# Optimization experiments

Hardware: AMD Instinct MI355X
Metric: run time of the kernel (lower is better)

The kernel has to match this reference:

```python
import jax, jax.numpy as jnp
import numpy as np

B, T, D_MODEL, N_HEADS, D_FF = 2, 2048, 512, 8, 2048
D_HEAD = D_MODEL // N_HEADS
EPS_LN = 1e-5
DEN_MIN = 1e-6


def setup_inputs() -> dict:
    key = jax.random.key(0)
    ks = jax.random.split(key, 12)
    def lin_w(k, din, dout):
        return jax.random.normal(k, (din, dout), jnp.float32) / np.sqrt(din).astype(np.float32)
    return {
        "x": jax.random.normal(ks[0], (B, T, D_MODEL), jnp.float32),
        "ln1_g": jnp.ones((D_MODEL,), jnp.float32),
        "ln1_b": jnp.zeros((D_MODEL,), jnp.float32),
        "Wq": lin_w(ks[1], D_MODEL, D_MODEL), "bq": jnp.zeros((D_MODEL,), jnp.float32),
        "Wk": lin_w(ks[2], D_MODEL, D_MODEL), "bk": jnp.zeros((D_MODEL,), jnp.float32),
        "Wv": lin_w(ks[3], D_MODEL, D_MODEL), "bv": jnp.zeros((D_MODEL,), jnp.float32),
        "Wo": lin_w(ks[4], D_MODEL, D_MODEL), "bo": jnp.zeros((D_MODEL,), jnp.float32),
        "ln2_g": jnp.ones((D_MODEL,), jnp.float32),
        "ln2_b": jnp.zeros((D_MODEL,), jnp.float32),
        "W1": lin_w(ks[5], D_MODEL, D_FF), "b1": jnp.zeros((D_FF,), jnp.float32),
        "W2": lin_w(ks[6], D_FF, D_MODEL), "b2": jnp.zeros((D_MODEL,), jnp.float32),
    }


def layer_norm(x, g, b):
    mu = jnp.mean(x, axis=-1, keepdims=True)
    var = jnp.var(x, axis=-1, keepdims=True)
    return (x - mu) * jax.lax.rsqrt(var + EPS_LN) * g + b


def causal_linear_attention(Q, K, V):
    # Q,K,V: (B,H,T,D); feature map already applied to Q,K.
    # Running summary S_t = cumsum_j phi(K_j) outer V_j, shape (B,H,T,D,D)
    KV = jnp.cumsum(K[..., :, None] * V[..., None, :], axis=2)
    z = jnp.cumsum(K, axis=2)                                   # (B,H,T,D)
    num = jnp.einsum('bhtd,bhtdm->bhtm', Q, KV)                 # (B,H,T,D)
    den = jnp.maximum(jnp.einsum('bhtd,bhtd->bht', Q, z), DEN_MIN)[..., None]
    return num / den


def reference(x, ln1_g, ln1_b, Wq, bq, Wk, bk, Wv, bv, Wo, bo,
              ln2_g, ln2_b, W1, b1, W2, b2):
    Bx, Tx, _ = x.shape
    # --- sublayer 1: pre-norm causal linear attention + residual ---
    h = layer_norm(x, ln1_g, ln1_b)
    def heads(y):  # (B,T,D_MODEL) -> (B,H,T,D_HEAD)
        return y.reshape(Bx, Tx, N_HEADS, D_HEAD).transpose(0, 2, 1, 3)
    Q = jax.nn.elu(heads(h @ Wq + bq)) + 1.0
    K = jax.nn.elu(heads(h @ Wk + bk)) + 1.0
    V = heads(h @ Wv + bv)
    attn = causal_linear_attention(Q, K, V)                     # (B,H,T,D)
    attn = attn.transpose(0, 2, 1, 3).reshape(Bx, Tx, D_MODEL)
    x = x + (attn @ Wo + bo)
    # --- sublayer 2: pre-norm FFN + residual (dropout=0, eval mode) ---
    h2 = layer_norm(x, ln2_g, ln2_b)
    ffn = jax.nn.relu(h2 @ W1 + b1) @ W2 + b2
    return x + ffn
```

## Files before the change

kernel.cpp:

```cpp
#include <hip/hip_runtime.h>
#include <hip/hip_bf16.h>
#include <cstdint>

#define T_SEQ   2048
#define DM      512
#define NH      8
#define DH      64
#define BATCH   2
#define MROWS   4096
#define DFF     2048
#define CHUNK   64
#define NCHUNK  32
#define BHN     16
#define ST_STRIDE 4160

typedef __attribute__((ext_vector_type(8))) short bf16x8;
typedef __attribute__((ext_vector_type(4))) float f32x4;
typedef __hip_bfloat16 bf16;

__device__ __forceinline__ void g2lds16(const bf16* g, bf16* l) {
    __builtin_amdgcn_global_load_lds(
        (const __attribute__((address_space(1))) unsigned int*)g,
        (__attribute__((address_space(3))) unsigned int*)l, 16, 0, 0);
}

__global__ __launch_bounds__(128) void ln_kernel(
    const float* __restrict__ x, const float* __restrict__ g,
    const float* __restrict__ b, bf16* __restrict__ y)
{
    int row = blockIdx.x;
    int t = threadIdx.x;
    const float4* xr = (const float4*)(x + (size_t)row * DM);
    float4 v = xr[t];
    float s  = v.x + v.y + v.z + v.w;
    float s2 = v.x*v.x + v.y*v.y + v.z*v.z + v.w*v.w;
#pragma unroll
    for (int off = 32; off > 0; off >>= 1) {
        s  += __shfl_down(s,  off);
        s2 += __shfl_down(s2, off);
    }
    __shared__ float sh[4];
    if ((t & 63) == 0) { sh[(t >> 6) * 2] = s; sh[(t >> 6) * 2 + 1] = s2; }
    __syncthreads();
    s  = sh[0] + sh[2];
    s2 = sh[1] + sh[3];
    float mu  = s * (1.0f / DM);
    float var = s2 * (1.0f / DM) - mu * mu;
    float rs  = rsqrtf(var + 1e-5f);
    float4 gg = ((const float4*)g)[t];
    float4 bb = ((const float4*)b)[t];
    union { short4 s4; bf16 h[4]; } u;
    u.h[0] = __float2bfloat16((v.x - mu) * rs * gg.x + bb.x);
    u.h[1] = __float2bfloat16((v.y - mu) * rs * gg.y + bb.y);
    u.h[2] = __float2bfloat16((v.z - mu) * rs * gg.z + bb.z);
    u.h[3] = __float2bfloat16((v.w - mu) * rs * gg.w + bb.w);
    *(short4*)(y + (size_t)row * DM + t * 4) = u.s4;
}

__global__ __launch_bounds__(256) void wcvt_all(
    const float* __restrict__ Wq, const float* __restrict__ Wk,
    const float* __restrict__ Wv, const float* __restrict__ Wo,
    const float* __restrict__ W1, const float* __restrict__ W2,
    bf16* __restrict__ QKVWT, bf16* __restrict__ WoT,
    bf16* __restrict__ W1T, bf16* __restrict__ W2T)
{
    __shared__ float tile[64][65];
    int bid = blockIdx.x;
    const float* src; bf16* dst; int K, N, txi, tyi;
    if (bid < 256) {
        int m = bid >> 6, t = bid & 63;
        src = m == 0 ? Wq : m == 1 ? Wk : m == 2 ? Wv : Wo;
        dst = m == 0 ? QKVWT : m == 1 ? QKVWT + 512*512
            : m == 2 ? QKVWT + 1024*512 : WoT;
        K = 512; N = 512; txi = t & 7; tyi = t >> 3;
    } else if (bid < 512) {
        int t = bid - 256;
        src = W1; dst = W1T; K = 512; N = 2048; txi = t & 31; tyi = t >> 5;
    } else {
        int t = bid - 512;
        src = W2; dst = W2T; K = 2048; N = 512; txi = t & 7; tyi = t >> 3;
    }
    int k0 = tyi * 64, n0 = txi * 64;
    int tid = threadIdx.x;
    int tr = tid >> 4, tc = (tid & 15) * 4;
#pragma unroll
    for (int i = 0; i < 4; i++) {
        float4 v = *(const float4*)(src + (size_t)(k0 + tr + i*16) * N + n0 + tc);
        tile[tr + i*16][tc+0] = v.x; tile[tr + i*16][tc+1] = v.y;
        tile[tr + i*16][tc+2] = v.z; tile[tr + i*16][tc+3] = v.w;
    }
    __syncthreads();
#pragma unroll
    for (int i = 0; i < 4; i++) {
        int n = tr + i*16;
        union { short4 s4; bf16 h[4]; } u;
#pragma unroll
        for (int j = 0; j < 4; j++) u.h[j] = __float2bfloat16(tile[tc+j][n]);
        *(short4*)(dst + (size_t)(n0 + n) * K + k0 + tc) = u.s4;
    }
}

template<int BM, int BN, int MODE>
__global__ __launch_bounds__(256) void mfma_gemm(
    const bf16* __restrict__ A, const bf16* __restrict__ Bt,
    const float* __restrict__ bias0, const float* __restrict__ bias1,
    const float* __restrict__ bias2, const float* __restrict__ res,
    float* __restrict__ outF,
    float* __restrict__ outQ, float* __restrict__ outK, float* __restrict__ outV,
    bf16* __restrict__ outB, int M, int N, int K)
{
    constexpr int BK = 64;
    constexpr int WTM = BM / 2, WTN = BN / 2;
    constexpr int FM = WTM / 16, FN = WTN / 16;
    __shared__ bf16 As[BM * BK];
    __shared__ bf16 Bs[BN * BK];
    const int tid = threadIdx.x;
    const int w = tid >> 6, lane = tid & 63;
    const int wr = w >> 1, wc = w & 1;
    const int bm0 = blockIdx.y * BM, bn0 = blockIdx.x * BN;
    const int srow = lane >> 3;
    const int scol = (lane & 7) * 8;

    f32x4 acc[FM][FN];
#pragma unroll
    for (int m = 0; m < FM; m++)
#pragma unroll
        for (int n = 0; n < FN; n++) acc[m][n] = (f32x4){0.f,0.f,0.f,0.f};

    for (int k0 = 0; k0 < K; k0 += BK) {
#pragma unroll
        for (int i = 0; i < BM/32; i++) {
            int c = i*4 + w;
            g2lds16(A + (size_t)(bm0 + c*8 + srow) * K + k0 + scol, &As[c*512]);
        }
#pragma unroll
        for (int i = 0; i < BN/32; i++) {
            int c = i*4 + w;
            g2lds16(Bt + (size_t)(bn0 + c*8 + srow) * K + k0 + scol, &Bs[c*512]);
        }
        __syncthreads();
#pragma unroll
        for (int kk = 0; kk < 2; kk++) {
            bf16x8 af[FM], bfr[FN];
#pragma unroll
            for (int m = 0; m < FM; m++)
                af[m] = *(const bf16x8*)&As[(wr*WTM + m*16 + (lane&15))*BK + kk*32 + (lane>>4)*8];
#pragma unroll
            for (int n = 0; n < FN; n++)
                bfr[n] = *(const bf16x8*)&Bs[(wc*WTN + n*16 + (lane&15))*BK + kk*32 + (lane>>4)*8];
#pragma unroll
            for (int m = 0; m < FM; m++)
#pragma unroll
                for (int n = 0; n < FN; n++)
                    acc[m][n] = __builtin_amdgcn_mfma_f32_16x16x32_bf16(af[m], bfr[n], acc[m][n], 0, 0, 0);
        }
        __syncthreads();
    }

    const int lr = (lane >> 4) * 4;
    const int lc = lane & 15;
#pragma unroll
    for (int m = 0; m < FM; m++) {
#pragma unroll
        for (int n = 0; n < FN; n++) {
            int col = bn0 + wc*WTN + n*16 + lc;
#pragma unroll
            for (int j = 0; j < 4; j++) {
                int r = bm0 + wr*WTM + m*16 + lr + j;
                float v = acc[m][n][j];
                if (MODE == 0) {
                    int which = col >> 9;
                    int cc = col & 511;
                    float bv_ = which == 0 ? bias0[cc] : which == 1 ? bias1[cc] : bias2[cc];
                    v += bv_;
                    if (which < 2) v = v > 0.f ? v + 1.f : __expf(v);
                    int hh = cc >> 6, dd = cc & 63;
                    int bb = r >> 11, tt = r & 2047;
                    float* dst = which == 0 ? outQ : which == 1 ? outK : outV;
                    dst[((((size_t)(bb*NH + hh)) * T_SEQ + tt) << 6) + dd] = v;
                } else if (MODE == 1) {
                    v += bias0[col] + res[(size_t)r * N + col];
                    outF[(size_t)r * N + col] = v;
                } else {
                    v += bias0[col];
                    v = fmaxf(v, 0.f);
                    outB[(size_t)r * N + col] = __float2bfloat16(v);
                }
            }
        }
    }
}

__global__ __launch_bounds__(256) void attn_chunk_sum(
    const float* __restrict__ Kb, const float* __restrict__ Vb,
    float* __restrict__ St)
{
    int blk = blockIdx.x;
    const float* Kp = Kb + (size_t)blk * (CHUNK * DH);
    const float* Vp = Vb + (size_t)blk * (CHUNK * DH);
    float* Sp = St + (size_t)blk * ST_STRIDE;
    __shared__ float Ks[64][64];
    __shared__ float Vs[64][64];
    int tid = threadIdx.x;
#pragma unroll
    for (int i = 0; i < 4; i++) {
        ((float4*)Ks)[tid + i*256] = ((const float4*)Kp)[tid + i*256];
        ((float4*)Vs)[tid + i*256] = ((const float4*)Vp)[tid + i*256];
    }
    __syncthreads();
    int r  = tid >> 2;
    int c0 = (tid & 3) * 16;
    float s[16];
#pragma unroll
    for (int i = 0; i < 16; i++) s[i] = 0.0f;
    for (int t = 0; t < 64; t++) {
        float kv = Ks[t][r];
        const float4* vr = (const float4*)&Vs[t][c0];
        float4 v0 = vr[0], v1 = vr[1], v2 = vr[2], v3 = vr[3];
        s[0]+=kv*v0.x; s[1]+=kv*v0.y; s[2]+=kv*v0.z; s[3]+=kv*v0.w;
        s[4]+=kv*v1.x; s[5]+=kv*v1.y; s[6]+=kv*v1.z; s[7]+=kv*v1.w;
        s[8]+=kv*v2.x; s[9]+=kv*v2.y; s[10]+=kv*v2.z; s[11]+=kv*v2.w;
        s[12]+=kv*v3.x; s[13]+=kv*v3.y; s[14]+=kv*v3.z; s[15]+=kv*v3.w;
    }
#pragma unroll
    for (int i = 0; i < 4; i++) {
        float4 ov = make_float4(s[i*4+0], s[i*4+1], s[i*4+2], s[i*4+3]);
        *(float4*)(Sp + (size_t)r*64 + c0 + i*4) = ov;
    }
    if (tid < 64) {
        float z = 0.0f;
        for (int t = 0; t < 64; t++) z += Ks[t][tid];
        Sp[4096 + tid] = z;
    }
}

__global__ __launch_bounds__(64) void attn_scan(float* __restrict__ St)
{
    int f4 = blockIdx.x * 64 + threadIdx.x;
    if (f4 >= ST_STRIDE / 4) return;
    int bh = blockIdx.y;
    float4* base = (float4*)(St + (size_t)bh * NCHUNK * ST_STRIDE) + f4;
    float4 run = make_float4(0.f, 0.f, 0.f, 0.f);
#pragma unroll 4
    for (int ch = 0; ch < NCHUNK; ch++) {
        float4* p = base + (size_t)ch * (ST_STRIDE / 4);
        float4 t = *p;
        *p = run;
        run.x += t.x; run.y += t.y; run.z += t.z; run.w += t.w;
    }
}

__global__ __launch_bounds__(256) void attn_out_k(
    const float* __restrict__ Qb, const float* __restrict__ Kb,
    const float* __restrict__ Vb, const float* __restrict__ St,
    bf16* __restrict__ attnb)
{
    int blk = blockIdx.x;
    int bh = blk >> 5, ch = blk & 31;
    int b = bh >> 3, h = bh & 7;
    const float* Qp = Qb + (size_t)blk * 4096;
    const float* Kp = Kb + (size_t)blk * 4096;
    const float* Vp = Vb + (size_t)blk * 4096;
    const float* Sp = St + (size_t)blk * ST_STRIDE;
    __shared__ float Qs[64][68];
    __shared__ float Kt[64][68];
    __shared__ float Vs[64][68];
    __shared__ float Ss[64][68];
    __shared__ float Amat[64][65];
    __shared__ float zs[64];
    int tid = threadIdx.x;
#pragma unroll
    for (int i = 0; i < 4; i++) {
        int fi = tid + i*256;
        int t  = fi >> 4;
        int d4 = (fi & 15) * 4;
        float4 q = ((const float4*)Qp)[fi];
        float4 k = ((const float4*)Kp)[fi];
        float4 v = ((const float4*)Vp)[fi];
        float4 s = ((const float4*)Sp)[fi];
        *(float4*)&Qs[t][d4] = q;
        *(float4*)&Vs[t][d4] = v;
        *(float4*)&Ss[t][d4] = s;
        Kt[d4+0][t] = k.x; Kt[d4+1][t] = k.y; Kt[d4+2][t] = k.z; Kt[d4+3][t] = k.w;
    }
    if (tid < 64) zs[tid] = Sp[4096 + tid];
    __syncthreads();
    int r  = tid >> 2;
    int c0 = (tid & 3) * 16;
    float a[16];
#pragma unroll
    for (int i = 0; i < 16; i++) a[i] = 0.0f;
    for (int d = 0; d < 64; d++) {
        float q = Qs[r][d];
        const float4* kr = (const float4*)&Kt[d][c0];
        float4 k0 = kr[0], k1 = kr[1], k2 = kr[2], k3 = kr[3];
        a[0]+=q*k0.x; a[1]+=q*k0.y; a[2]+=q*k0.z; a[3]+=q*k0.w;
        a[4]+=q*k1.x; a[5]+=q*k1.y; a[6]+=q*k1.z; a[7]+=q*k1.w;
        a[8]+=q*k2.x; a[9]+=q*k2.y; a[10]+=q*k2.z; a[11]+=q*k2.w;
        a[12]+=q*k3.x; a[13]+=q*k3.y; a[14]+=q*k3.z; a[15]+=q*k3.w;
    }
#pragma unroll
    for (int i = 0; i < 16; i++) Amat[r][c0+i] = a[i];
    __syncthreads();
    float den = 0.0f;
    for (int d = 0; d < 64; d++) den += Qs[r][d] * zs[d];
    for (int j = 0; j <= r; j++) den += Amat[r][j];
    den = fmaxf(den, 1e-6f);
    float num[16];
#pragma unroll
    for (int i = 0; i < 16; i++) num[i] = 0.0f;
    for (int d = 0; d < 64; d++) {
        float q = Qs[r][d];
        const float4* sv = (const float4*)&Ss[d][c0];
        float4 s0 = sv[0], s1 = sv[1], s2 = sv[2], s3 = sv[3];
        num[0]+=q*s0.x; num[1]+=q*s0.y; num[2]+=q*s0.z; num[3]+=q*s0.w;
        num[4]+=q*s1.x; num[5]+=q*s1.y; num[6]+=q*s1.z; num[7]+=q*s1.w;
        num[8]+=q*s2.x; num[9]+=q*s2.y; num[10]+=q*s2.z; num[11]+=q*s2.w;
        num[12]+=q*s3.x; num[13]+=q*s3.y; num[14]+=q*s3.z; num[15]+=q*s3.w;
    }
    for (int j = 0; j <= r; j++) {
        float aj = Amat[r][j];
        const float4* vv = (const float4*)&Vs[j][c0];
        float4 v0 = vv[0], v1 = vv[1], v2 = vv[2], v3 = vv[3];
        num[0]+=aj*v0.x; num[1]+=aj*v0.y; num[2]+=aj*v0.z; num[3]+=aj*v0.w;
        num[4]+=aj*v1.x; num[5]+=aj*v1.y; num[6]+=aj*v1.z; num[7]+=aj*v1.w;
        num[8]+=aj*v2.x; num[9]+=aj*v2.y; num[10]+=aj*v2.z; num[11]+=aj*v2.w;
        num[12]+=aj*v3.x; num[13]+=aj*v3.y; num[14]+=aj*v3.z; num[15]+=aj*v3.w;
    }
    float inv = 1.0f / den;
    union { short4 s4[4]; bf16 hh[16]; } u;
#pragma unroll
    for (int i = 0; i < 16; i++) u.hh[i] = __float2bfloat16(num[i] * inv);
    short4* op = (short4*)(attnb + ((size_t)b * T_SEQ + ch*64 + r) * DM + h*64 + c0);
#pragma unroll
    for (int i = 0; i < 4; i++) op[i] = u.s4[i];
}

extern "C" void kernel_launch(void* const* d_in, const int* in_sizes, int n_in,
                              void* d_out, int out_size, void* d_ws, size_t ws_size,
                              hipStream_t stream)
{
    (void)in_sizes; (void)n_in; (void)out_size; (void)ws_size;
    const float* x     = (const float*)d_in[0];
    const float* ln1_g = (const float*)d_in[1];
    const float* ln1_b = (const float*)d_in[2];
    const float* Wq = (const float*)d_in[3];
    const float* bq = (const float*)d_in[4];
    const float* Wk = (const float*)d_in[5];
    const float* bk = (const float*)d_in[6];
    const float* Wv = (const float*)d_in[7];
    const float* bv = (const float*)d_in[8];
    const float* Wo = (const float*)d_in[9];
    const float* bo = (const float*)d_in[10];
    const float* ln2_g = (const float*)d_in[11];
    const float* ln2_b = (const float*)d_in[12];
    const float* W1 = (const float*)d_in[13];
    const float* b1 = (const float*)d_in[14];
    const float* W2 = (const float*)d_in[15];
    const float* b2 = (const float*)d_in[16];
    float* out = (float*)d_out;
    char* base = (char*)d_ws;

    bf16*  h_bf  = (bf16*)(base + 0);
    bf16*  h2_bf = (bf16*)(base + 4194304);
    bf16*  attnb = (bf16*)(base + 8388608);
    bf16*  QKVWT = (bf16*)(base + 12582912);
    bf16*  WoT   = (bf16*)(base + 14155776);
    bf16*  W1T   = (bf16*)(base + 14680064);
    bf16*  W2T   = (bf16*)(base + 16777216);
    float* Qb    = (float*)(base + 18874368);
    float* Kb    = (float*)(base + 27262976);
    float* Vb    = (float*)(base + 35651584);
    float* St    = (float*)(base + 44040192);
    float* X2    = (float*)(base + 52559872);
    bf16*  FF    = (bf16*)(base + 60948480);

    wcvt_all<<<768, 256, 0, stream>>>(Wq, Wk, Wv, Wo, W1, W2,
                                      QKVWT, WoT, W1T, W2T);

    ln_kernel<<<MROWS, 128, 0, stream>>>(x, ln1_g, ln1_b, h_bf);

    mfma_gemm<128,128,0><<<dim3(12, 32), 256, 0, stream>>>(
        h_bf, QKVWT, bq, bk, bv, nullptr, nullptr, Qb, Kb, Vb, nullptr,
        MROWS, 1536, 512);

    attn_chunk_sum<<<BHN*NCHUNK, 256, 0, stream>>>(Kb, Vb, St);
    attn_scan<<<dim3(17, BHN), 64, 0, stream>>>(St);
    attn_out_k<<<BHN*NCHUNK, 256, 0, stream>>>(Qb, Kb, Vb, St, attnb);

    mfma_gemm<64,128,1><<<dim3(4, 64), 256, 0, stream>>>(
        attnb, WoT, bo, nullptr, nullptr, x, X2, nullptr, nullptr, nullptr, nullptr,
        MROWS, 512, 512);

    ln_kernel<<<MROWS, 128, 0, stream>>>(X2, ln2_g, ln2_b, h2_bf);

    mfma_gemm<128,128,2><<<dim3(16, 32), 256, 0, stream>>>(
        h2_bf, W1T, b1, nullptr, nullptr, nullptr, nullptr, nullptr, nullptr, nullptr, FF,
        MROWS, DFF, 512);

    mfma_gemm<64,128,1><<<dim3(4, 64), 256, 0, stream>>>(
        FF, W2T, b2, nullptr, nullptr, X2, out, nullptr, nullptr, nullptr, nullptr,
        MROWS, 512, DFF);
}
```

Measured before the change: 233.0 us.

## Split-K final FFN GEMM with atomics, retile GEMMs with configurable wave layouts

The GEMM template now takes a configurable wave grid, so the QKV and W1 GEMMs run with 8 waves (512 threads) and the Wo GEMM uses 64x64 tiles to launch more blocks. The W2 GEMM is split along K into two halves and accumulates into the output with atomic adds. The second layernorm kernel pre-initialises the output with residual plus b2 so those atomics can land on it. This aims to raise occupancy and block count on the small-N GEMMs, at the cost of atomic traffic and floating-point summation that is no longer deterministic.

After: 228.7 us. About the same (-1.9%).

```diff
diff --git a/kernel.cpp b/kernel.cpp
--- a/kernel.cpp
+++ b/kernel.cpp
@@ -24,9 +24,11 @@
         (__attribute__((address_space(3))) unsigned int*)l, 16, 0, 0);
 }
 
+template<bool INIT>
 __global__ __launch_bounds__(128) void ln_kernel(
     const float* __restrict__ x, const float* __restrict__ g,
-    const float* __restrict__ b, bf16* __restrict__ y)
+    const float* __restrict__ b, bf16* __restrict__ y,
+    const float* __restrict__ b2, float* __restrict__ oinit)
 {
     int row = blockIdx.x;
     int t = threadIdx.x;
@@ -55,6 +57,11 @@
     u.h[2] = __float2bfloat16((v.z - mu) * rs * gg.z + bb.z);
     u.h[3] = __float2bfloat16((v.w - mu) * rs * gg.w + bb.w);
     *(short4*)(y + (size_t)row * DM + t * 4) = u.s4;
+    if (INIT) {
+        float4 b2v = ((const float4*)b2)[t];
+        float4 ov = make_float4(v.x + b2v.x, v.y + b2v.y, v.z + b2v.z, v.w + b2v.w);
+        ((float4*)(oinit + (size_t)row * DM))[t] = ov;
+    }
 }
 
 __global__ __launch_bounds__(256) void wcvt_all(
@@ -100,8 +107,8 @@
     }
 }
 
-template<int BM, int BN, int MODE>
-__global__ __launch_bounds__(256) void mfma_gemm(
+template<int BM, int BN, int WM, int WN, int MODE>
+__global__ __launch_bounds__(WM*WN*64) void mfma_gemm(
     const bf16* __restrict__ A, const bf16* __restrict__ Bt,
     const float* __restrict__ bias0, const float* __restrict__ bias1,
     const float* __restrict__ bias2, const float* __restrict__ res,
@@ -110,32 +117,37 @@
     bf16* __restrict__ outB, int M, int N, int K)
 {
     constexpr int BK = 64;
-    constexpr int WTM = BM / 2, WTN = BN / 2;
+    constexpr int WAVES = WM * WN;
+    constexpr int WTM = BM / WM, WTN = BN / WN;
     constexpr int FM = WTM / 16, FN = WTN / 16;
+    constexpr int IA = BM / 8 / WAVES, IB = BN / 8 / WAVES;
     __shared__ bf16 As[BM * BK];
     __shared__ bf16 Bs[BN * BK];
     const int tid = threadIdx.x;
     const int w = tid >> 6, lane = tid & 63;
-    const int wr = w >> 1, wc = w & 1;
+    const int wr = w / WN, wc = w % WN;
     const int bm0 = blockIdx.y * BM, bn0 = blockIdx.x * BN;
     const int srow = lane >> 3;
     const int scol = (lane & 7) * 8;
 
+    int kbeg = 0, kend = K;
+    if (MODE == 3) { int half = K >> 1; kbeg = blockIdx.z * half; kend = kbeg + half; }
+
     f32x4 acc[FM][FN];
 #pragma unroll
     for (int m = 0; m < FM; m++)
 #pragma unroll
         for (int n = 0; n < FN; n++) acc[m][n] = (f32x4){0.f,0.f,0.f,0.f};
 
-    for (int k0 = 0; k0 < K; k0 += BK) {
-#pragma unroll
-        for (int i = 0; i < BM/32; i++) {
-            int c = i*4 + w;
+    for (int k0 = kbeg; k0 < kend; k0 += BK) {
+#pragma unroll
+        for (int i = 0; i < IA; i++) {
+            int c = i*WAVES + w;
             g2lds16(A + (size_t)(bm0 + c*8 + srow) * K + k0 + scol, &As[c*512]);
         }
 #pragma unroll
-        for (int i = 0; i < BN/32; i++) {
-            int c = i*4 + w;
+        for (int i = 0; i < IB; i++) {
+            int c = i*WAVES + w;
             g2lds16(Bt + (size_t)(bn0 + c*8 + srow) * K + k0 + scol, &Bs[c*512]);
         }
         __syncthreads();
@@ -181,10 +193,12 @@
                 } else if (MODE == 1) {
                     v += bias0[col] + res[(size_t)r * N + col];
                     outF[(size_t)r * N + col] = v;
-                } else {
+                } else if (MODE == 2) {
                     v += bias0[col];
                     v = fmaxf(v, 0.f);
                     outB[(size_t)r * N + col] = __float2bfloat16(v);
+                } else {
+                    unsafeAtomicAdd(&outF[(size_t)r * N + col], v);
                 }
             }
         }
@@ -378,9 +392,9 @@
     wcvt_all<<<768, 256, 0, stream>>>(Wq, Wk, Wv, Wo, W1, W2,
                                       QKVWT, WoT, W1T, W2T);
 
-    ln_kernel<<<MROWS, 128, 0, stream>>>(x, ln1_g, ln1_b, h_bf);
-
-    mfma_gemm<128,128,0><<<dim3(12, 32), 256, 0, stream>>>(
+    ln_kernel<false><<<MROWS, 128, 0, stream>>>(x, ln1_g, ln1_b, h_bf, nullptr, nullptr);
+
+    mfma_gemm<128,128,4,2,0><<<dim3(12, 32), 512, 0, stream>>>(
         h_bf, QKVWT, bq, bk, bv, nullptr, nullptr, Qb, Kb, Vb, nullptr,
         MROWS, 1536, 512);
 
@@ -388,17 +402,17 @@
     attn_scan<<<dim3(17, BHN), 64, 0, stream>>>(St);
     attn_out_k<<<BHN*NCHUNK, 256, 0, stream>>>(Qb, Kb, Vb, St, attnb);
 
-    mfma_gemm<64,128,1><<<dim3(4, 64), 256, 0, stream>>>(
+    mfma_gemm<64,64,2,2,1><<<dim3(8, 64), 256, 0, stream>>>(
         attnb, WoT, bo, nullptr, nullptr, x, X2, nullptr, nullptr, nullptr, nullptr,
         MROWS, 512, 512);
 
-    ln_kernel<<<MROWS, 128, 0, stream>>>(X2, ln2_g, ln2_b, h2_bf);
-
-    mfma_gemm<128,128,2><<<dim3(16, 32), 256, 0, stream>>>(
+    ln_kernel<true><<<MROWS, 128, 0, stream>>>(X2, ln2_g, ln2_b, h2_bf, b2, out);
+
+    mfma_gemm<128,128,4,2,2><<<dim3(16, 32), 512, 0, stream>>>(
         h2_bf, W1T, b1, nullptr, nullptr, nullptr, nullptr, nullptr, nullptr, nullptr, FF,
         MROWS, DFF, 512);
 
-    mfma_gemm<64,128,1><<<dim3(4, 64), 256, 0, stream>>>(
-        FF, W2T, b2, nullptr, nullptr, X2, out, nullptr, nullptr, nullptr, nullptr,
-        MROWS, 512, DFF);
-}
+    mfma_gemm<128,64,2,2,3><<<dim3(8, 32, 2), 256, 0, stream>>>(
+        FF, W2T, nullptr, nullptr, nullptr, nullptr, out, nullptr, nullptr, nullptr, nullptr,
+        MROWS, 512, 2048);
+}
```
